# Kernel optimization log

Measured on AMD Instinct MI355X. Metric: run time of the kernel, lower is better.

Reference implementation:

```python
import jax, jax.numpy as jnp
import numpy as np

# dims from QBN_GRU_Base.__init__ with in_dim=64
IN_DIM = 64
OBS_MID = 28   # int(abs(64 - 8) / 2)
OBS_BN = 8
M_SIZE = 16
LATENT = 16
M_BN = 8
T, B = 512, 2048


def _lin_params(key, out_d, in_d):
    # normc init: normal(0,1) rows scaled to unit L2 norm, zero bias
    w = jax.random.normal(key, (out_d, in_d), dtype=jnp.float32)
    w = w / jnp.sqrt(jnp.sum(w * w, axis=1, keepdims=True))
    b = jnp.zeros((out_d,), dtype=jnp.float32)
    return w, b


def setup_inputs() -> dict:
    key = jax.random.key(0)
    ks = jax.random.split(key, 16)
    x = jax.random.normal(ks[0], (T, B, IN_DIM), dtype=jnp.float32)
    obs_w0, obs_b0 = _lin_params(ks[1], OBS_MID, IN_DIM)
    obs_w1, obs_b1 = _lin_params(ks[2], OBS_MID, OBS_MID)
    obs_w2, obs_b2 = _lin_params(ks[3], OBS_BN, OBS_MID)
    s = float(1.0 / np.sqrt(M_SIZE))  # torch GRUCell default init
    gru_wih = jax.random.uniform(ks[4], (3 * M_SIZE, OBS_BN), jnp.float32, -s, s)
    gru_whh = jax.random.uniform(ks[5], (3 * M_SIZE, M_SIZE), jnp.float32, -s, s)
    gru_bih = jax.random.uniform(ks[6], (3 * M_SIZE,), jnp.float32, -s, s)
    gru_bhh = jax.random.uniform(ks[7], (3 * M_SIZE,), jnp.float32, -s, s)
    m2q_w0, m2q_b0 = _lin_params(ks[8], LATENT, M_SIZE)
    m2q_w1, m2q_b1 = _lin_params(ks[9], LATENT, LATENT)
    m2q_w2, m2q_b2 = _lin_params(ks[10], M_BN, LATENT)
    q2m_w0, q2m_b0 = _lin_params(ks[11], LATENT, M_BN)
    q2m_w1, q2m_b1 = _lin_params(ks[12], LATENT, LATENT)
    q2m_w2, q2m_b2 = _lin_params(ks[13], M_SIZE, LATENT)
    act_w, act_b = _lin_params(ks[14], LATENT, M_SIZE)
    return dict(x=x,
                obs_w0=obs_w0, obs_b0=obs_b0, obs_w1=obs_w1, obs_b1=obs_b1,
                obs_w2=obs_w2, obs_b2=obs_b2,
                gru_wih=gru_wih, gru_whh=gru_whh, gru_bih=gru_bih, gru_bhh=gru_bhh,
                m2q_w0=m2q_w0, m2q_b0=m2q_b0, m2q_w1=m2q_w1, m2q_b1=m2q_b1,
                m2q_w2=m2q_w2, m2q_b2=m2q_b2,
                q2m_w0=q2m_w0, q2m_b0=q2m_b0, q2m_w1=q2m_w1, q2m_b1=q2m_b1,
                q2m_w2=q2m_w2, q2m_b2=q2m_b2,
                act_w=act_w, act_b=act_b)


def _ternary_tanh(v):
    # QBN soft ternary activation with straight-through rounding to {-1,0,1}
    soft = 1.5 * jnp.tanh(v) + 0.5 * jnp.tanh(-3.0 * v)
    return soft + jax.lax.stop_gradient(jnp.round(soft) - soft)


def reference(x, obs_w0, obs_b0, obs_w1, obs_b1, obs_w2, obs_b2,
              gru_wih, gru_whh, gru_bih, gru_bhh,
              m2q_w0, m2q_b0, m2q_w1, m2q_b1, m2q_w2, m2q_b2,
              q2m_w0, q2m_b0, q2m_w1, q2m_b1, q2m_w2, q2m_b2,
              act_w, act_b):
    # observation QBN encoder, applied to all timesteps at once [T,B,in]->[T,B,8]
    h = jnp.tanh(x @ obs_w0.T + obs_b0)
    h = jnp.tanh(h @ obs_w1.T + obs_b1)
    xq = _ternary_tanh(h @ obs_w2.T + obs_b2)

    def step(hid, x_t):
        # torch.nn.GRUCell math
        gi = x_t @ gru_wih.T + gru_bih        # [B, 3*M]
        gh = hid @ gru_whh.T + gru_bhh
        ir, iz, inn = jnp.split(gi, 3, axis=-1)
        hr, hz, hn = jnp.split(gh, 3, axis=-1)
        r = jax.nn.sigmoid(ir + hr)
        z = jax.nn.sigmoid(iz + hz)
        n = jnp.tanh(inn + r * hn)
        ht = (1.0 - z) * n + z * hid
        # memory -> quantized bottleneck
        q = jnp.tanh(ht @ m2q_w0.T + m2q_b0)
        q = jnp.tanh(q @ m2q_w1.T + m2q_b1)
        q = _ternary_tanh(q @ m2q_w2.T + m2q_b2)
        # bottleneck -> memory (all layers tanh)
        m = jnp.tanh(q @ q2m_w0.T + q2m_b0)
        m = jnp.tanh(m @ q2m_w1.T + q2m_b1)
        m = jnp.tanh(m @ q2m_w2.T + q2m_b2)
        return m, m  # new hidden, and per-step output y

    h0 = jnp.zeros((x.shape[1], M_SIZE), dtype=x.dtype)
    _, ys = jax.lax.scan(step, h0, xq)        # [T, B, M_SIZE]
    return jnp.tanh(ys @ act_w.T + act_b)     # action latent [T, B, LATENT]
```

## Files before the change

kernel.cpp:

```cpp
#include <hip/hip_runtime.h>


#define T_DIM 512
#define B_DIM 2048
#define NELEM (T_DIM * B_DIM)

__device__ __forceinline__ float tanh_xla(float x) {
  const float kClamp = 7.99881172180175781f;
  float xc = fminf(fmaxf(x, -kClamp), kClamp);
  float x2 = xc * xc;
  float p = fmaf(x2, -2.76076847742355e-16f, 2.00018790482477e-13f);
  p = fmaf(x2, p, -8.60467152213735e-11f);
  p = fmaf(x2, p, 5.12229709037114e-08f);
  p = fmaf(x2, p, 1.48572235717979e-05f);
  p = fmaf(x2, p, 6.37261928875436e-04f);
  p = fmaf(x2, p, 4.89352455891786e-03f);
  p = xc * p;
  float q = fmaf(x2, 1.19825839466702e-06f, 1.18534705686654e-04f);
  q = fmaf(x2, q, 2.26843463243900e-03f);
  q = fmaf(x2, q, 4.89352518554385e-03f);
  float r = p / q;
  return (fabsf(x) < 0.0004f) ? x : r;
}

__device__ __forceinline__ float sigmoid_xla(float x) {
  return 0.5f + 0.5f * tanh_xla(0.5f * x);
}

__device__ __forceinline__ float soft_ternary(float v) {
  return 1.5f * tanh_xla(v) + 0.5f * tanh_xla(-3.0f * v);
}

__device__ __forceinline__ int ternary_digit(float v) {
  return (int)rintf(soft_ternary(v)) + 1;
}

__global__ void k_thr(float* __restrict__ thr) {
  if (threadIdx.x == 0 && blockIdx.x == 0) {
    float lo = 0.0f, hi = 4.0f;
    for (int i = 0; i < 64; ++i) {
      float mid = 0.5f * (lo + hi);
      if (rintf(soft_ternary(mid)) >= 1.0f) hi = mid; else lo = mid;
    }
    thr[0] = hi;
  }
}

__global__ __launch_bounds__(256)
__attribute__((amdgpu_waves_per_eu(1, 4)))
void k_obs(
    const float* __restrict__ x,
    const float* __restrict__ w0, const float* __restrict__ b0,
    const float* __restrict__ w1, const float* __restrict__ b1,
    const float* __restrict__ w2, const float* __restrict__ b2,
    unsigned short* __restrict__ xcodes) {
  int e = blockIdx.x * 256 + threadIdx.x;
  const float* xr = x + (size_t)e * 64;
  float xv[64];
#pragma unroll
  for (int j = 0; j < 64; j += 4) {
    float4 v = *reinterpret_cast<const float4*>(xr + j);
    xv[j] = v.x; xv[j + 1] = v.y; xv[j + 2] = v.z; xv[j + 3] = v.w;
  }
  float h1[28];
#pragma unroll
  for (int k = 0; k < 28; ++k) {
    float acc = 0.0f;
#pragma unroll
    for (int j = 0; j < 64; ++j) acc = fmaf(w0[k * 64 + j], xv[j], acc);
    h1[k] = tanh_xla(acc + b0[k]);
  }
  float h2[28];
#pragma unroll
  for (int k = 0; k < 28; ++k) {
    float acc = 0.0f;
#pragma unroll
    for (int j = 0; j < 28; ++j) acc = fmaf(w1[k * 28 + j], h1[j], acc);
    h2[k] = tanh_xla(acc + b1[k]);
  }
  const int p3[8] = {1, 3, 9, 27, 81, 243, 729, 2187};
  unsigned code = 0;
#pragma unroll
  for (int k = 0; k < 8; ++k) {
    float acc = 0.0f;
#pragma unroll
    for (int j = 0; j < 28; ++j) acc = fmaf(w2[k * 28 + j], h2[j], acc);
    code += (unsigned)(ternary_digit(acc + b2[k]) * p3[k]);
  }
  xcodes[e] = (unsigned short)code;
}

__global__ __launch_bounds__(256) void k_gi(
    const float* __restrict__ wih, const float* __restrict__ bih,
    float* __restrict__ gip) {
  int c = blockIdx.x * 256 + threadIdx.x;
  if (c >= 6561) return;
  float q[8];
  unsigned cc = (unsigned)c;
#pragma unroll
  for (int k = 0; k < 8; ++k) { q[k] = (float)((int)(cc % 3u) - 1); cc /= 3u; }
#pragma unroll
  for (int i = 0; i < 16; ++i) {
    float gr = 0.f, gz = 0.f, gn = 0.f;
#pragma unroll
    for (int j = 0; j < 8; ++j) {
      gr = fmaf(wih[i * 8 + j], q[j], gr);
      gz = fmaf(wih[(16 + i) * 8 + j], q[j], gz);
      gn = fmaf(wih[(32 + i) * 8 + j], q[j], gn);
    }
    float4 o;
    o.x = gr + bih[i]; o.y = gz + bih[16 + i]; o.z = gn + bih[32 + i]; o.w = 0.f;
    *reinterpret_cast<float4*>(gip + (size_t)c * 64 + i * 4) = o;
  }
}

__global__ __launch_bounds__(256) void k_mtab(
    const float* __restrict__ q2m_w0, const float* __restrict__ q2m_b0,
    const float* __restrict__ q2m_w1, const float* __restrict__ q2m_b1,
    const float* __restrict__ q2m_w2, const float* __restrict__ q2m_b2,
    const float* __restrict__ whh, const float* __restrict__ bhh,
    const float* __restrict__ act_w, const float* __restrict__ act_b,
    float* __restrict__ ghm, float* __restrict__ ytab) {
  int c = blockIdx.x * 256 + threadIdx.x;
  if (c > 6561) return;
  float m[16];
  if (c == 6561) {
#pragma unroll
    for (int i = 0; i < 16; ++i) m[i] = 0.0f;
  } else {
    float q[8];
    unsigned cc = (unsigned)c;
#pragma unroll
    for (int k = 0; k < 8; ++k) { q[k] = (float)((int)(cc % 3u) - 1); cc /= 3u; }
    float a[16];
#pragma unroll
    for (int i = 0; i < 16; ++i) {
      float acc = 0.f;
#pragma unroll
      for (int j = 0; j < 8; ++j) acc = fmaf(q2m_w0[i * 8 + j], q[j], acc);
      a[i] = tanh_xla(acc + q2m_b0[i]);
    }
    float d[16];
#pragma unroll
    for (int i = 0; i < 16; ++i) {
      float acc = 0.f;
#pragma unroll
      for (int j = 0; j < 16; ++j) acc = fmaf(q2m_w1[i * 16 + j], a[j], acc);
      d[i] = tanh_xla(acc + q2m_b1[i]);
    }
#pragma unroll
    for (int i = 0; i < 16; ++i) {
      float acc = 0.f;
#pragma unroll
      for (int j = 0; j < 16; ++j) acc = fmaf(q2m_w2[i * 16 + j], d[j], acc);
      m[i] = tanh_xla(acc + q2m_b2[i]);
    }
  }
#pragma unroll
  for (int i = 0; i < 16; ++i) {
    float gr = 0.f, gz = 0.f, gn = 0.f;
#pragma unroll
    for (int j = 0; j < 16; ++j) {
      gr = fmaf(whh[i * 16 + j], m[j], gr);
      gz = fmaf(whh[(16 + i) * 16 + j], m[j], gz);
      gn = fmaf(whh[(32 + i) * 16 + j], m[j], gn);
    }
    float4 o;
    o.x = gr + bhh[i]; o.y = gz + bhh[16 + i]; o.z = gn + bhh[32 + i]; o.w = m[i];
    *reinterpret_cast<float4*>(ghm + (size_t)c * 64 + i * 4) = o;
  }
  if (c < 6561) {
#pragma unroll
    for (int i = 0; i < 16; ++i) {
      float acc = 0.f;
#pragma unroll
      for (int j = 0; j < 16; ++j) acc = fmaf(act_w[i * 16 + j], m[j], acc);
      ytab[(size_t)c * 16 + i] = tanh_xla(acc + act_b[i]);
    }
  }
}

__device__ __forceinline__ void bperm16(int base4, float v, float* o) {
  asm volatile(
      "ds_bpermute_b32 %0, %16, %17 offset:0\n\t"
      "ds_bpermute_b32 %1, %16, %17 offset:4\n\t"
      "ds_bpermute_b32 %2, %16, %17 offset:8\n\t"
      "ds_bpermute_b32 %3, %16, %17 offset:12\n\t"
      "ds_bpermute_b32 %4, %16, %17 offset:16\n\t"
      "ds_bpermute_b32 %5, %16, %17 offset:20\n\t"
      "ds_bpermute_b32 %6, %16, %17 offset:24\n\t"
      "ds_bpermute_b32 %7, %16, %17 offset:28\n\t"
      "ds_bpermute_b32 %8, %16, %17 offset:32\n\t"
      "ds_bpermute_b32 %9, %16, %17 offset:36\n\t"
      "ds_bpermute_b32 %10, %16, %17 offset:40\n\t"
      "ds_bpermute_b32 %11, %16, %17 offset:44\n\t"
      "ds_bpermute_b32 %12, %16, %17 offset:48\n\t"
      "ds_bpermute_b32 %13, %16, %17 offset:52\n\t"
      "ds_bpermute_b32 %14, %16, %17 offset:56\n\t"
      "ds_bpermute_b32 %15, %16, %17 offset:60\n\t"
      "s_waitcnt lgkmcnt(0)"
      : "=&v"(o[0]), "=&v"(o[1]), "=&v"(o[2]), "=&v"(o[3]),
        "=&v"(o[4]), "=&v"(o[5]), "=&v"(o[6]), "=&v"(o[7]),
        "=&v"(o[8]), "=&v"(o[9]), "=&v"(o[10]), "=&v"(o[11]),
        "=&v"(o[12]), "=&v"(o[13]), "=&v"(o[14]), "=&v"(o[15])
      : "v"(base4), "v"(v));
}

#define PIN8(a, b, c, d, e, f, g, h)                                        \
  asm volatile("" : "+v"(a), "+v"(b), "+v"(c), "+v"(d), "+v"(e), "+v"(f),   \
                    "+v"(g), "+v"(h))

#define DPP_ROR_ADD(v, CTRL)                                               \
  v += __int_as_float(__builtin_amdgcn_update_dpp(                         \
      0, __float_as_int(v), (CTRL), 0xF, 0xF, true))

__global__ __launch_bounds__(64)
__attribute__((amdgpu_waves_per_eu(1, 1)))
void k_scan(
    const unsigned short* __restrict__ xcodes,
    const float* __restrict__ ghm,
    const float* __restrict__ gip,
    const float* __restrict__ m2q_w0, const float* __restrict__ m2q_b0,
    const float* __restrict__ m2q_w1, const float* __restrict__ m2q_b1,
    const float* __restrict__ m2q_w2, const float* __restrict__ m2q_b2,
    const float* __restrict__ thr,
    unsigned short* __restrict__ qcodes) {
  int lane = threadIdx.x & 15;
  int b = (blockIdx.x * 64 + threadIdx.x) >> 4;
  int base4 = (threadIdx.x & 48) << 2;
  int lane16 = lane * 16;

  float w0r[16], w1r[16], w2r[16];
#pragma unroll
  for (int j = 0; j < 16; j += 4) {
    float4 a = *reinterpret_cast<const float4*>(m2q_w0 + lane * 16 + j);
    w0r[j] = a.x; w0r[j + 1] = a.y; w0r[j + 2] = a.z; w0r[j + 3] = a.w;
    float4 bq = *reinterpret_cast<const float4*>(m2q_w1 + lane * 16 + j);
    w1r[j] = bq.x; w1r[j + 1] = bq.y; w1r[j + 2] = bq.z; w1r[j + 3] = bq.w;
    float4 cq = *reinterpret_cast<const float4*>(m2q_w2 + (lane & 7) * 16 + j);
    w2r[j] = cq.x; w2r[j + 1] = cq.y; w2r[j + 2] = cq.z; w2r[j + 3] = cq.w;
  }
  float b0l = m2q_b0[lane], b1l = m2q_b1[lane], b2l = m2q_b2[lane & 7];
  int p3i = 1;
  for (int k = 0; k < (lane & 7); ++k) p3i *= 3;
  float w3f = (lane < 8) ? (float)(p3i * 256) : 0.0f;
  float thi = thr[0];
  const int kOffBias = 3280 * 256;

  PIN8(w0r[0], w0r[1], w0r[2], w0r[3], w0r[4], w0r[5], w0r[6], w0r[7]);
  PIN8(w0r[8], w0r[9], w0r[10], w0r[11], w0r[12], w0r[13], w0r[14], w0r[15]);
  PIN8(w1r[0], w1r[1], w1r[2], w1r[3], w1r[4], w1r[5], w1r[6], w1r[7]);
  PIN8(w1r[8], w1r[9], w1r[10], w1r[11], w1r[12], w1r[13], w1r[14], w1r[15]);
  PIN8(w2r[0], w2r[1], w2r[2], w2r[3], w2r[4], w2r[5], w2r[6], w2r[7]);
  PIN8(w2r[8], w2r[9], w2r[10], w2r[11], w2r[12], w2r[13], w2r[14], w2r[15]);
  asm volatile("" : "+v"(b0l), "+v"(b1l), "+v"(b2l), "+v"(w3f), "+v"(thi));

  const char* ghmB = (const char*)ghm;
  const char* gipB = (const char*)gip;

  int qoff = 6561 * 256;
  unsigned xc = xcodes[b];
  float4 i4 = *reinterpret_cast<const float4*>(gipB + (unsigned)(((int)xc << 8) + lane16));

  for (int t = 0; t < T_DIM; ++t) {
    float4 g4 = *reinterpret_cast<const float4*>(ghmB + (unsigned)(qoff + lane16));
    int tn = (t + 1) & (T_DIM - 1);
    unsigned xcn = xcodes[tn * B_DIM + b];
    float4 i4n = *reinterpret_cast<const float4*>(gipB + (unsigned)(((int)xcn << 8) + lane16));

    float r = sigmoid_xla(i4.x + g4.x);
    float z = sigmoid_xla(i4.y + g4.y);
    float n = tanh_xla(fmaf(r, g4.z, i4.z));
    float h = (1.0f - z) * n + z * g4.w;

    float hv[16];
    bperm16(base4, h, hv);
    float acc = 0.f;
#pragma unroll
    for (int j = 0; j < 16; ++j) acc = fmaf(w0r[j], hv[j], acc);
    float t0 = tanh_xla(acc + b0l);

    float tv0[16];
    bperm16(base4, t0, tv0);
    acc = 0.f;
#pragma unroll
    for (int j = 0; j < 16; ++j) acc = fmaf(w1r[j], tv0[j], acc);
    float t1 = tanh_xla(acc + b1l);

    float tv1[16];
    bperm16(base4, t1, tv1);
    acc = 0.f;
#pragma unroll
    for (int j = 0; j < 16; ++j) acc = fmaf(w2r[j], tv1[j], acc);

    float s = acc + b2l;
    float df = (s >= thi) ? 1.0f : ((s <= -thi) ? -1.0f : 0.0f);
    if (__builtin_expect(__any(fabsf(fabsf(s) - thi) < 1e-3f), 0)) {
      df = rintf(soft_ternary(s));
    }
    float st = df * w3f;
    DPP_ROR_ADD(st, 0x128);
    DPP_ROR_ADD(st, 0x124);
    DPP_ROR_ADD(st, 0x122);
    DPP_ROR_ADD(st, 0x121);
    qoff = (int)st + kOffBias;

    if (lane == 0) qcodes[t * B_DIM + b] = (unsigned short)((unsigned)qoff >> 8);
    i4 = i4n;
  }
}

__global__ __launch_bounds__(256) void k_out(
    const unsigned short* __restrict__ qcodes,
    const float* __restrict__ ytab,
    float* __restrict__ out) {
  int i = blockIdx.x * 256 + threadIdx.x;
  int e = i >> 2, sub = i & 3;
  unsigned c = qcodes[e];
  float4 y = *reinterpret_cast<const float4*>(ytab + (size_t)c * 16 + sub * 4);
  reinterpret_cast<float4*>(out)[i] = y;
}

extern "C" void kernel_launch(void* const* d_in, const int* in_sizes, int n_in,
                              void* d_out, int out_size, void* d_ws, size_t ws_size,
                              hipStream_t stream) {
  (void)in_sizes; (void)n_in; (void)out_size; (void)ws_size;
  const float* x       = (const float*)d_in[0];
  const float* obs_w0  = (const float*)d_in[1];
  const float* obs_b0  = (const float*)d_in[2];
  const float* obs_w1  = (const float*)d_in[3];
  const float* obs_b1  = (const float*)d_in[4];
  const float* obs_w2  = (const float*)d_in[5];
  const float* obs_b2  = (const float*)d_in[6];
  const float* gru_wih = (const float*)d_in[7];
  const float* gru_whh = (const float*)d_in[8];
  const float* gru_bih = (const float*)d_in[9];
  const float* gru_bhh = (const float*)d_in[10];
  const float* m2q_w0  = (const float*)d_in[11];
  const float* m2q_b0  = (const float*)d_in[12];
  const float* m2q_w1  = (const float*)d_in[13];
  const float* m2q_b1  = (const float*)d_in[14];
  const float* m2q_w2  = (const float*)d_in[15];
  const float* m2q_b2  = (const float*)d_in[16];
  const float* q2m_w0  = (const float*)d_in[17];
  const float* q2m_b0  = (const float*)d_in[18];
  const float* q2m_w1  = (const float*)d_in[19];
  const float* q2m_b1  = (const float*)d_in[20];
  const float* q2m_w2  = (const float*)d_in[21];
  const float* q2m_b2  = (const float*)d_in[22];
  const float* act_w   = (const float*)d_in[23];
  const float* act_b   = (const float*)d_in[24];

  char* ws = (char*)d_ws;
  unsigned short* xcodes = (unsigned short*)(ws);
  unsigned short* qcodes = (unsigned short*)(ws + (2u << 20));
  float* gip  = (float*)(ws + (4u << 20));
  float* ghm  = (float*)(ws + (6u << 20));
  float* ytab = (float*)(ws + (8u << 20));
  float* thr  = (float*)(ws + (8u << 20) + (512u << 10));

  k_thr<<<1, 64, 0, stream>>>(thr);
  k_gi<<<26, 256, 0, stream>>>(gru_wih, gru_bih, gip);
  k_mtab<<<26, 256, 0, stream>>>(q2m_w0, q2m_b0, q2m_w1, q2m_b1, q2m_w2, q2m_b2,
                                 gru_whh, gru_bhh, act_w, act_b, ghm, ytab);
  k_obs<<<NELEM / 256, 256, 0, stream>>>(x, obs_w0, obs_b0, obs_w1, obs_b1,
                                         obs_w2, obs_b2, xcodes);
  k_scan<<<(B_DIM * 16) / 64, 64, 0, stream>>>(xcodes, ghm, gip,
                                               m2q_w0, m2q_b0, m2q_w1, m2q_b1,
                                               m2q_w2, m2q_b2, thr, qcodes);
  k_out<<<(NELEM * 4) / 256, 256, 0, stream>>>(qcodes, ytab, (float*)d_out);
}
```

Before: 1.046 ms.

## Use rcp-based tanh with exact fallback near ternary thresholds in obs and scan

Replaces the exact-division tanh with a reciprocal-instruction variant in both the observation MLP and the recurrent scan. Ternary quantization is done by comparing against a precomputed threshold, and the exact path is recomputed only when a value falls near that threshold. k_obs also restructures the first layer to accumulate while streaming x in float4 chunks, and drops the waves_per_eu hint. The goal is to cut the divide cost and the per-element soft-ternary work on the critical path. The cost is larger code from the rarely taken fallback branches, plus some register pressure.

```diff
diff --git a/kernel.cpp b/kernel.cpp
--- a/kernel.cpp
+++ b/kernel.cpp
@@ -23,8 +23,30 @@
   return (fabsf(x) < 0.0004f) ? x : r;
 }
 
+__device__ __forceinline__ float tanh_fast(float x) {
+  const float kClamp = 7.99881172180175781f;
+  float xc = fminf(fmaxf(x, -kClamp), kClamp);
+  float x2 = xc * xc;
+  float p = fmaf(x2, -2.76076847742355e-16f, 2.00018790482477e-13f);
+  p = fmaf(x2, p, -8.60467152213735e-11f);
+  p = fmaf(x2, p, 5.12229709037114e-08f);
+  p = fmaf(x2, p, 1.48572235717979e-05f);
+  p = fmaf(x2, p, 6.37261928875436e-04f);
+  p = fmaf(x2, p, 4.89352455891786e-03f);
+  p = xc * p;
+  float q = fmaf(x2, 1.19825839466702e-06f, 1.18534705686654e-04f);
+  q = fmaf(x2, q, 2.26843463243900e-03f);
+  q = fmaf(x2, q, 4.89352518554385e-03f);
+  float rq;
+  asm("v_rcp_f32 %0, %1" : "=v"(rq) : "v"(q));
+  return p * rq;
+}
+
 __device__ __forceinline__ float sigmoid_xla(float x) {
   return 0.5f + 0.5f * tanh_xla(0.5f * x);
+}
+__device__ __forceinline__ float sigmoid_fast(float x) {
+  return 0.5f + 0.5f * tanh_fast(0.5f * x);
 }
 
 __device__ __forceinline__ float soft_ternary(float v) {
@@ -46,46 +68,89 @@
   }
 }
 
-__global__ __launch_bounds__(256)
-__attribute__((amdgpu_waves_per_eu(1, 4)))
-void k_obs(
+__global__ __launch_bounds__(256) void k_obs(
     const float* __restrict__ x,
     const float* __restrict__ w0, const float* __restrict__ b0,
     const float* __restrict__ w1, const float* __restrict__ b1,
     const float* __restrict__ w2, const float* __restrict__ b2,
+    const float* __restrict__ thr,
     unsigned short* __restrict__ xcodes) {
   int e = blockIdx.x * 256 + threadIdx.x;
   const float* xr = x + (size_t)e * 64;
-  float xv[64];
+  float th = thr[0];
+  const int p3[8] = {1, 3, 9, 27, 81, 243, 729, 2187};
+
+  float a1[28];
+#pragma unroll
+  for (int k = 0; k < 28; ++k) a1[k] = 0.0f;
 #pragma unroll
   for (int j = 0; j < 64; j += 4) {
     float4 v = *reinterpret_cast<const float4*>(xr + j);
-    xv[j] = v.x; xv[j + 1] = v.y; xv[j + 2] = v.z; xv[j + 3] = v.w;
+#pragma unroll
+    for (int k = 0; k < 28; ++k) {
+      a1[k] = fmaf(w0[k * 64 + j + 0], v.x, a1[k]);
+      a1[k] = fmaf(w0[k * 64 + j + 1], v.y, a1[k]);
+      a1[k] = fmaf(w0[k * 64 + j + 2], v.z, a1[k]);
+      a1[k] = fmaf(w0[k * 64 + j + 3], v.w, a1[k]);
+    }
   }
   float h1[28];
+#pragma unroll
+  for (int k = 0; k < 28; ++k) h1[k] = tanh_fast(a1[k] + b0[k]);
+  float h2[28];
 #pragma unroll
   for (int k = 0; k < 28; ++k) {
     float acc = 0.0f;
 #pragma unroll
-    for (int j = 0; j < 64; ++j) acc = fmaf(w0[k * 64 + j], xv[j], acc);
-    h1[k] = tanh_xla(acc + b0[k]);
-  }
-  float h2[28];
-#pragma unroll
-  for (int k = 0; k < 28; ++k) {
-    float acc = 0.0f;
-#pragma unroll
     for (int j = 0; j < 28; ++j) acc = fmaf(w1[k * 28 + j], h1[j], acc);
-    h2[k] = tanh_xla(acc + b1[k]);
-  }
-  const int p3[8] = {1, 3, 9, 27, 81, 243, 729, 2187};
+    h2[k] = tanh_fast(acc + b1[k]);
+  }
   unsigned code = 0;
+  bool bad = false;
 #pragma unroll
   for (int k = 0; k < 8; ++k) {
     float acc = 0.0f;
 #pragma unroll
     for (int j = 0; j < 28; ++j) acc = fmaf(w2[k * 28 + j], h2[j], acc);
-    code += (unsigned)(ternary_digit(acc + b2[k]) * p3[k]);
+    float s = acc + b2[k];
+    bad = bad || (fabsf(fabsf(s) - th) < 1e-4f);
+    int d = (s >= th) ? 2 : ((s <= -th) ? 0 : 1);
+    code += (unsigned)(d * p3[k]);
+  }
+  if (__builtin_expect(bad, 0)) {
+    float e1[28];
+#pragma unroll
+    for (int k = 0; k < 28; ++k) e1[k] = 0.0f;
+#pragma unroll
+    for (int j = 0; j < 64; j += 4) {
+      float4 v = *reinterpret_cast<const float4*>(xr + j);
+#pragma unroll
+      for (int k = 0; k < 28; ++k) {
+        e1[k] = fmaf(w0[k * 64 + j + 0], v.x, e1[k]);
+        e1[k] = fmaf(w0[k * 64 + j + 1], v.y, e1[k]);
+        e1[k] = fmaf(w0[k * 64 + j + 2], v.z, e1[k]);
+        e1[k] = fmaf(w0[k * 64 + j + 3], v.w, e1[k]);
+      }
+    }
+    float g1[28];
+#pragma unroll
+    for (int k = 0; k < 28; ++k) g1[k] = tanh_xla(e1[k] + b0[k]);
+    float g2[28];
+#pragma unroll
+    for (int k = 0; k < 28; ++k) {
+      float acc = 0.0f;
+#pragma unroll
+      for (int j = 0; j < 28; ++j) acc = fmaf(w1[k * 28 + j], g1[j], acc);
+      g2[k] = tanh_xla(acc + b1[k]);
+    }
+    code = 0;
+#pragma unroll
+    for (int k = 0; k < 8; ++k) {
+      float acc = 0.0f;
+#pragma unroll
+      for (int j = 0; j < 28; ++j) acc = fmaf(w2[k * 28 + j], g2[j], acc);
+      code += (unsigned)(ternary_digit(acc + b2[k]) * p3[k]);
+    }
   }
   xcodes[e] = (unsigned short)code;
 }
@@ -268,9 +333,9 @@
     unsigned xcn = xcodes[tn * B_DIM + b];
     float4 i4n = *reinterpret_cast<const float4*>(gipB + (unsigned)(((int)xcn << 8) + lane16));
 
-    float r = sigmoid_xla(i4.x + g4.x);
-    float z = sigmoid_xla(i4.y + g4.y);
-    float n = tanh_xla(fmaf(r, g4.z, i4.z));
+    float r = sigmoid_fast(i4.x + g4.x);
+    float z = sigmoid_fast(i4.y + g4.y);
+    float n = tanh_fast(fmaf(r, g4.z, i4.z));
     float h = (1.0f - z) * n + z * g4.w;
 
     float hv[16];
@@ -278,14 +343,14 @@
     float acc = 0.f;
 #pragma unroll
     for (int j = 0; j < 16; ++j) acc = fmaf(w0r[j], hv[j], acc);
-    float t0 = tanh_xla(acc + b0l);
+    float t0 = tanh_fast(acc + b0l);
 
     float tv0[16];
     bperm16(base4, t0, tv0);
     acc = 0.f;
 #pragma unroll
     for (int j = 0; j < 16; ++j) acc = fmaf(w1r[j], tv0[j], acc);
-    float t1 = tanh_xla(acc + b1l);
+    float t1 = tanh_fast(acc + b1l);
 
     float tv1[16];
     bperm16(base4, t1, tv1);
@@ -296,7 +361,29 @@
     float s = acc + b2l;
     float df = (s >= thi) ? 1.0f : ((s <= -thi) ? -1.0f : 0.0f);
     if (__builtin_expect(__any(fabsf(fabsf(s) - thi) < 1e-3f), 0)) {
-      df = rintf(soft_ternary(s));
+      float re = sigmoid_xla(i4.x + g4.x);
+      float ze = sigmoid_xla(i4.y + g4.y);
+      float ne = tanh_xla(fmaf(re, g4.z, i4.z));
+      float he = (1.0f - ze) * ne + ze * g4.w;
+      float hve[16];
+      bperm16(base4, he, hve);
+      acc = 0.f;
+#pragma unroll
+      for (int j = 0; j < 16; ++j) acc = fmaf(w0r[j], hve[j], acc);
+      float t0e = tanh_xla(acc + b0l);
+      float tv0e[16];
+      bperm16(base4, t0e, tv0e);
+      acc = 0.f;
+#pragma unroll
+      for (int j = 0; j < 16; ++j) acc = fmaf(w1r[j], tv0e[j], acc);
+      float t1e = tanh_xla(acc + b1l);
+      float tv1e[16];
+      bperm16(base4, t1e, tv1e);
+      acc = 0.f;
+#pragma unroll
+      for (int j = 0; j < 16; ++j) acc = fmaf(w2r[j], tv1e[j], acc);
+      float se = acc + b2l;
+      df = rintf(soft_ternary(se));
     }
     float st = df * w3f;
     DPP_ROR_ADD(st, 0x128);
@@ -364,7 +451,7 @@
   k_mtab<<<26, 256, 0, stream>>>(q2m_w0, q2m_b0, q2m_w1, q2m_b1, q2m_w2, q2m_b2,
                                  gru_whh, gru_bhh, act_w, act_b, ghm, ytab);
   k_obs<<<NELEM / 256, 256, 0, stream>>>(x, obs_w0, obs_b0, obs_w1, obs_b1,
-                                         obs_w2, obs_b2, xcodes);
+                                         obs_w2, obs_b2, thr, xcodes);
   k_scan<<<(B_DIM * 16) / 64, 64, 0, stream>>>(xcodes, ghm, gip,
                                                m2q_w0, m2q_b0, m2q_w1, m2q_b1,
                                                m2q_w2, m2q_b2, thr, qcodes);
```

New measurement: 1.164 ms. 1.11x slower.
